# Kernel tuning notes

Hardware: AMD Instinct MI355X
Metric: run time of the kernel (lower is better)

Reference implementation:

```python
import jax, jax.numpy as jnp
import numpy as np

NUM_NODES = 8192
IN_FEATURES = 1024
OUT_FEATURES = 512
NUM_EDGES = 262144  # avg degree 32


def setup_inputs() -> dict:
    key = jax.random.key(0)
    k_x, k_w, k_b, k_src, k_dst = jax.random.split(key, 5)
    x = jax.random.normal(k_x, (NUM_NODES, IN_FEATURES), dtype=jnp.float32)
    # torch nn.Linear layout: weight [out, in], bias [out]
    W = jax.random.normal(k_w, (OUT_FEATURES, IN_FEATURES), dtype=jnp.float32) * (1.0 / np.sqrt(IN_FEATURES))
    b = jax.random.normal(k_b, (OUT_FEATURES,), dtype=jnp.float32) * 0.01
    src = jax.random.randint(k_src, (NUM_EDGES,), 0, NUM_NODES, dtype=jnp.int64)
    dst = jax.random.randint(k_dst, (NUM_EDGES,), 0, NUM_NODES, dtype=jnp.int64)
    edge_index = jnp.stack([src, dst], axis=0)
    return {"x": x, "W": W, "b": b, "edge_index": edge_index, "num_nodes": NUM_NODES}


def reference(x, W, b, edge_index, num_nodes):
    # Faithful to the torch module: build dense adjacency from edge list
    # (duplicate edges collapse to 1.0 via assignment semantics),
    # linear, (dropout p=0 -> identity), dense adj @ hidden, relu.
    adj = jnp.zeros((num_nodes, num_nodes), dtype=x.dtype)
    adj = adj.at[edge_index[0], edge_index[1]].set(1.0)
    hidden = x @ W.T + b            # [N, out]
    support = adj @ hidden          # [N, out] aggregation over neighbors
    return jax.nn.relu(support)
```

## Files before the change

### kernel.cpp

```cpp
#include <hip/hip_runtime.h>

#define N_NODES 8192
#define IN_F    1024
#define OUT_F   512
#define N_EDGES 262144
#define STRIDE  96

#define HID_OFF     0u
#define XB_OFF      8388608u
#define WB_OFF      25165824u
#define DEG_OFF     26214400u
#define COL_OFF     26247168u
#define MAX_DEG     STRIDE

typedef short  bf16x8 __attribute__((ext_vector_type(8)));
typedef float  f32x4  __attribute__((ext_vector_type(4)));

__device__ __forceinline__ unsigned short f2bf(float f) {
    unsigned u = __float_as_uint(f);
    u += 0x7fffu + ((u >> 16) & 1u);
    return (unsigned short)(u >> 16);
}

__device__ __forceinline__ void ld_lds16(const void* g, void* l) {
    __builtin_amdgcn_global_load_lds(
        (const __attribute__((address_space(1))) void*)g,
        (__attribute__((address_space(3))) void*)l, 16, 0, 0);
}

#define NX8 (N_NODES * IN_F / 8)
#define NW8 (OUT_F * IN_F / 8)
__global__ __launch_bounds__(256) void cvt_bf16_all(const float* __restrict__ x,
                                                    const float* __restrict__ w,
                                                    unsigned short* __restrict__ xb,
                                                    int* __restrict__ deg) {
    int i = blockIdx.x * blockDim.x + threadIdx.x;
    if (i < N_NODES) deg[i] = 0;
    if (i >= NX8 + NW8) return;
    const float4* p = (i < NX8) ? ((const float4*)x + (size_t)i * 2)
                                : ((const float4*)w + (size_t)(i - NX8) * 2);
    float4 v0 = p[0], v1 = p[1];
    uint4 o;
    o.x = (unsigned)f2bf(v0.x) | ((unsigned)f2bf(v0.y) << 16);
    o.y = (unsigned)f2bf(v0.z) | ((unsigned)f2bf(v0.w) << 16);
    o.z = (unsigned)f2bf(v1.x) | ((unsigned)f2bf(v1.y) << 16);
    o.w = (unsigned)f2bf(v1.z) | ((unsigned)f2bf(v1.w) << 16);
    *((uint4*)xb + i) = o;
}

__global__ __launch_bounds__(256, 4) void gemm_mfma(const unsigned short* __restrict__ Xb,
                                                    const unsigned short* __restrict__ Wb,
                                                    const float* __restrict__ bias,
                                                    unsigned short* __restrict__ H) {
    __shared__ unsigned short As[64 * 32];
    __shared__ unsigned short Bs[64 * 32];

    const int tid  = threadIdx.x;
    const int lane = tid & 63;
    const int wave = tid >> 6;
    const int row0 = blockIdx.x * 64;
    const int col0 = blockIdx.y * 64;
    const int wm   = (wave & 1) * 32;
    const int wn   = (wave >> 1) * 32;
    const int fm   = lane & 15;
    const int fk   = (lane >> 4) * 8;

    f32x4 acc[2][2];
#pragma unroll
    for (int i = 0; i < 2; ++i)
#pragma unroll
        for (int j = 0; j < 2; ++j) acc[i][j] = (f32x4)0.f;

    const int r0 = tid >> 2, kc0 = (tid & 3) * 8;

    for (int k0 = 0; k0 < IN_F; k0 += 32) {
        ld_lds16(Xb + (size_t)(row0 + r0) * IN_F + k0 + kc0, As + tid * 8);
        ld_lds16(Wb + (size_t)(col0 + r0) * IN_F + k0 + kc0, Bs + tid * 8);
        __syncthreads();

        bf16x8 a[2], b[2];
#pragma unroll
        for (int mi = 0; mi < 2; ++mi)
            a[mi] = *(const bf16x8*)&As[(wm + mi * 16 + fm) * 32 + fk];
#pragma unroll
        for (int ni = 0; ni < 2; ++ni)
            b[ni] = *(const bf16x8*)&Bs[(wn + ni * 16 + fm) * 32 + fk];
#pragma unroll
        for (int mi = 0; mi < 2; ++mi)
#pragma unroll
            for (int ni = 0; ni < 2; ++ni)
                acc[mi][ni] = __builtin_amdgcn_mfma_f32_16x16x32_bf16(
                    a[mi], b[ni], acc[mi][ni], 0, 0, 0);
        __syncthreads();
    }

    const int cm = (lane >> 4) * 4;
#pragma unroll
    for (int ni = 0; ni < 2; ++ni) {
        const int col = col0 + wn + ni * 16 + fm;
        const float bv = bias[col];
#pragma unroll
        for (int mi = 0; mi < 2; ++mi) {
#pragma unroll
            for (int r = 0; r < 4; ++r) {
                const int row = row0 + wm + mi * 16 + cm + r;
                H[(size_t)row * OUT_F + col] = f2bf(acc[mi][ni][r] + bv);
            }
        }
    }
}

__global__ void scatter_direct(const int* __restrict__ src, const int* __restrict__ dst,
                               int* __restrict__ deg, int* __restrict__ col) {
    int e = blockIdx.x * blockDim.x + threadIdx.x;
    if (e >= N_EDGES) return;
    int s = src[e];
    int slot = atomicAdd(&deg[s], 1);
    if (slot < STRIDE) col[s * STRIDE + slot] = dst[e];
}

__global__ __launch_bounds__(256) void aggregate(const unsigned short* __restrict__ H,
                                                 const int* __restrict__ dg,
                                                 const int* __restrict__ col,
                                                 float* __restrict__ out) {
    __shared__ int   nbr[MAX_DEG];
    __shared__ int   uniq[MAX_DEG];
    __shared__ float part[4 * OUT_F];
    __shared__ int   lcnt;
    const int v    = blockIdx.x;
    const int tid  = threadIdx.x;
    const int wave = tid >> 6;
    const int lane = tid & 63;
    int deg = dg[v];
    if (deg > MAX_DEG) deg = MAX_DEG;

    if (tid == 0) lcnt = 0;
    for (int i = tid; i < deg; i += 256) nbr[i] = col[v * STRIDE + i];
    __syncthreads();
    for (int i = tid; i < deg; i += 256) {
        int d = nbr[i];
        bool dup = false;
        for (int j = 0; j < i; ++j)
            if (nbr[j] == d) { dup = true; break; }
        if (!dup) uniq[atomicAdd(&lcnt, 1)] = d;
    }
    __syncthreads();
    const int n  = lcnt;
    const int f0 = lane * 8;

    float a0=0,a1=0,a2=0,a3=0,a4=0,a5=0,a6=0,a7=0;
    int e = wave;
    for (; e + 4 < n; e += 8) {
        uint4 h0 = *(const uint4*)&H[(size_t)uniq[e]     * OUT_F + f0];
        uint4 h1 = *(const uint4*)&H[(size_t)uniq[e + 4] * OUT_F + f0];
        a0 += __uint_as_float(h0.x << 16) + __uint_as_float(h1.x << 16);
        a1 += __uint_as_float(h0.x & 0xffff0000u) + __uint_as_float(h1.x & 0xffff0000u);
        a2 += __uint_as_float(h0.y << 16) + __uint_as_float(h1.y << 16);
        a3 += __uint_as_float(h0.y & 0xffff0000u) + __uint_as_float(h1.y & 0xffff0000u);
        a4 += __uint_as_float(h0.z << 16) + __uint_as_float(h1.z << 16);
        a5 += __uint_as_float(h0.z & 0xffff0000u) + __uint_as_float(h1.z & 0xffff0000u);
        a6 += __uint_as_float(h0.w << 16) + __uint_as_float(h1.w << 16);
        a7 += __uint_as_float(h0.w & 0xffff0000u) + __uint_as_float(h1.w & 0xffff0000u);
    }
    for (; e < n; e += 4) {
        uint4 h0 = *(const uint4*)&H[(size_t)uniq[e] * OUT_F + f0];
        a0 += __uint_as_float(h0.x << 16);
        a1 += __uint_as_float(h0.x & 0xffff0000u);
        a2 += __uint_as_float(h0.y << 16);
        a3 += __uint_as_float(h0.y & 0xffff0000u);
        a4 += __uint_as_float(h0.z << 16);
        a5 += __uint_as_float(h0.z & 0xffff0000u);
        a6 += __uint_as_float(h0.w << 16);
        a7 += __uint_as_float(h0.w & 0xffff0000u);
    }
    float4 p0 = {a0, a1, a2, a3}, p1 = {a4, a5, a6, a7};
    *(float4*)&part[wave * OUT_F + f0]     = p0;
    *(float4*)&part[wave * OUT_F + f0 + 4] = p1;
    __syncthreads();

    const int f = tid * 2;
    float sx = part[0 * OUT_F + f]     + part[1 * OUT_F + f]
             + part[2 * OUT_F + f]     + part[3 * OUT_F + f];
    float sy = part[0 * OUT_F + f + 1] + part[1 * OUT_F + f + 1]
             + part[2 * OUT_F + f + 1] + part[3 * OUT_F + f + 1];
    float2 o;
    o.x = fmaxf(sx, 0.f);
    o.y = fmaxf(sy, 0.f);
    *(float2*)&out[(size_t)v * OUT_F + f] = o;
}

extern "C" void kernel_launch(void* const* d_in, const int* in_sizes, int n_in,
                              void* d_out, int out_size, void* d_ws, size_t ws_size,
                              hipStream_t stream) {
    const float* x  = (const float*)d_in[0];
    const float* W  = (const float*)d_in[1];
    const float* b  = (const float*)d_in[2];
    const int*   ei = (const int*)d_in[3];
    float* out = (float*)d_out;

    char* ws = (char*)d_ws;
    unsigned short* H   = (unsigned short*)(ws + HID_OFF);
    unsigned short* Xb  = (unsigned short*)(ws + XB_OFF);
    unsigned short* Wb  = (unsigned short*)(ws + WB_OFF);
    int*            deg = (int*)(ws + DEG_OFF);
    int*            col = (int*)(ws + COL_OFF);

    cvt_bf16_all<<<(NX8 + NW8 + 255) / 256, 256, 0, stream>>>(x, W, Xb, deg);

    scatter_direct<<<(N_EDGES + 255) / 256, 256, 0, stream>>>(ei, ei + N_EDGES, deg, col);

    gemm_mfma<<<dim3(N_NODES / 64, OUT_F / 64), 256, 0, stream>>>(Xb, Wb, b, H);

    aggregate<<<N_NODES, 256, 0, stream>>>(H, deg, col, out);
}
```

Measured before the change: 154.7 us.

## Fuse edge scatter into GEMM launch and use one wave per node in aggregation

The edge scatter is merged into the GEMM kernel as extra blocks (block ids 1024 and above) on a 1D grid, removing one kernel launch and letting the atomics overlap with MFMA work. The aggregation kernel now assigns one node per wavefront instead of one per block. This replaces block-wide barriers and the LDS cross-wave reduction with wave barriers, and deduplication runs per wave. The risk is less memory-level parallelism per node, with each wave walking all its neighbours serially, plus GEMM and scatter blocks competing for the same compute units.

```diff
diff --git a/kernel.cpp b/kernel.cpp
--- a/kernel.cpp
+++ b/kernel.cpp
@@ -21,6 +21,9 @@
     u += 0x7fffu + ((u >> 16) & 1u);
     return (unsigned short)(u >> 16);
 }
+
+__device__ __forceinline__ float bflo(unsigned u) { return __uint_as_float(u << 16); }
+__device__ __forceinline__ float bfhi(unsigned u) { return __uint_as_float(u & 0xffff0000u); }
 
 __device__ __forceinline__ void ld_lds16(const void* g, void* l) {
     __builtin_amdgcn_global_load_lds(
@@ -48,18 +51,32 @@
     *((uint4*)xb + i) = o;
 }
 
-__global__ __launch_bounds__(256, 4) void gemm_mfma(const unsigned short* __restrict__ Xb,
-                                                    const unsigned short* __restrict__ Wb,
-                                                    const float* __restrict__ bias,
-                                                    unsigned short* __restrict__ H) {
+__global__ __launch_bounds__(256, 4) void gemm_scatter(const unsigned short* __restrict__ Xb,
+                                                       const unsigned short* __restrict__ Wb,
+                                                       const float* __restrict__ bias,
+                                                       unsigned short* __restrict__ H,
+                                                       const int* __restrict__ src,
+                                                       const int* __restrict__ dst,
+                                                       int* __restrict__ deg,
+                                                       int* __restrict__ col) {
     __shared__ unsigned short As[64 * 32];
     __shared__ unsigned short Bs[64 * 32];
 
-    const int tid  = threadIdx.x;
+    const int bid = blockIdx.x;
+    const int tid = threadIdx.x;
+
+    if (bid >= 1024) {
+        int e = (bid - 1024) * 256 + tid;
+        int s = src[e];
+        int slot = atomicAdd(&deg[s], 1);
+        if (slot < STRIDE) col[s * STRIDE + slot] = dst[e];
+        return;
+    }
+
     const int lane = tid & 63;
     const int wave = tid >> 6;
-    const int row0 = blockIdx.x * 64;
-    const int col0 = blockIdx.y * 64;
+    const int row0 = (bid & 127) * 64;
+    const int col0 = (bid >> 7) * 64;
     const int wm   = (wave & 1) * 32;
     const int wn   = (wave >> 1) * 32;
     const int fm   = lane & 15;
@@ -97,96 +114,79 @@
     const int cm = (lane >> 4) * 4;
 #pragma unroll
     for (int ni = 0; ni < 2; ++ni) {
-        const int col = col0 + wn + ni * 16 + fm;
-        const float bv = bias[col];
+        const int c = col0 + wn + ni * 16 + fm;
+        const float bv = bias[c];
 #pragma unroll
         for (int mi = 0; mi < 2; ++mi) {
 #pragma unroll
             for (int r = 0; r < 4; ++r) {
                 const int row = row0 + wm + mi * 16 + cm + r;
-                H[(size_t)row * OUT_F + col] = f2bf(acc[mi][ni][r] + bv);
+                H[(size_t)row * OUT_F + c] = f2bf(acc[mi][ni][r] + bv);
             }
         }
     }
-}
-
-__global__ void scatter_direct(const int* __restrict__ src, const int* __restrict__ dst,
-                               int* __restrict__ deg, int* __restrict__ col) {
-    int e = blockIdx.x * blockDim.x + threadIdx.x;
-    if (e >= N_EDGES) return;
-    int s = src[e];
-    int slot = atomicAdd(&deg[s], 1);
-    if (slot < STRIDE) col[s * STRIDE + slot] = dst[e];
 }
 
 __global__ __launch_bounds__(256) void aggregate(const unsigned short* __restrict__ H,
                                                  const int* __restrict__ dg,
                                                  const int* __restrict__ col,
                                                  float* __restrict__ out) {
-    __shared__ int   nbr[MAX_DEG];
-    __shared__ int   uniq[MAX_DEG];
-    __shared__ float part[4 * OUT_F];
-    __shared__ int   lcnt;
-    const int v    = blockIdx.x;
-    const int tid  = threadIdx.x;
-    const int wave = tid >> 6;
-    const int lane = tid & 63;
-    int deg = dg[v];
-    if (deg > MAX_DEG) deg = MAX_DEG;
-
-    if (tid == 0) lcnt = 0;
-    for (int i = tid; i < deg; i += 256) nbr[i] = col[v * STRIDE + i];
-    __syncthreads();
-    for (int i = tid; i < deg; i += 256) {
-        int d = nbr[i];
-        bool dup = false;
-        for (int j = 0; j < i; ++j)
-            if (nbr[j] == d) { dup = true; break; }
-        if (!dup) uniq[atomicAdd(&lcnt, 1)] = d;
-    }
-    __syncthreads();
-    const int n  = lcnt;
+    __shared__ int nbr[4][MAX_DEG];
+    __shared__ int uniq[4][MAX_DEG];
+    __shared__ int wcnt[4];
+    const int wave = threadIdx.x >> 6;
+    const int lane = threadIdx.x & 63;
+    const int v    = blockIdx.x * 4 + wave;
+    int d = dg[v];
+    if (d > MAX_DEG) d = MAX_DEG;
+
+    if (lane == 0) wcnt[wave] = 0;
+    int id0 = -1, id1 = -1;
+    if (lane < d)      { id0 = col[v * STRIDE + lane];      nbr[wave][lane]      = id0; }
+    if (64 + lane < d) { id1 = col[v * STRIDE + 64 + lane]; nbr[wave][64 + lane] = id1; }
+    __builtin_amdgcn_wave_barrier();
+
+    bool k0 = (lane < d);
+    const int lim0 = k0 ? lane : 0;
+    for (int j = 0; j < lim0; ++j) k0 = k0 & (nbr[wave][j] != id0);
+    bool k1 = (64 + lane < d);
+    const int lim1 = k1 ? (64 + lane) : 0;
+    for (int j = 0; j < lim1; ++j) k1 = k1 & (nbr[wave][j] != id1);
+    if (k0) uniq[wave][atomicAdd(&wcnt[wave], 1)] = id0;
+    if (k1) uniq[wave][atomicAdd(&wcnt[wave], 1)] = id1;
+    __builtin_amdgcn_wave_barrier();
+    const int n  = wcnt[wave];
     const int f0 = lane * 8;
 
     float a0=0,a1=0,a2=0,a3=0,a4=0,a5=0,a6=0,a7=0;
-    int e = wave;
-    for (; e + 4 < n; e += 8) {
-        uint4 h0 = *(const uint4*)&H[(size_t)uniq[e]     * OUT_F + f0];
-        uint4 h1 = *(const uint4*)&H[(size_t)uniq[e + 4] * OUT_F + f0];
-        a0 += __uint_as_float(h0.x << 16) + __uint_as_float(h1.x << 16);
-        a1 += __uint_as_float(h0.x & 0xffff0000u) + __uint_as_float(h1.x & 0xffff0000u);
-        a2 += __uint_as_float(h0.y << 16) + __uint_as_float(h1.y << 16);
-        a3 += __uint_as_float(h0.y & 0xffff0000u) + __uint_as_float(h1.y & 0xffff0000u);
-        a4 += __uint_as_float(h0.z << 16) + __uint_as_float(h1.z << 16);
-        a5 += __uint_as_float(h0.z & 0xffff0000u) + __uint_as_float(h1.z & 0xffff0000u);
-        a6 += __uint_as_float(h0.w << 16) + __uint_as_float(h1.w << 16);
-        a7 += __uint_as_float(h0.w & 0xffff0000u) + __uint_as_float(h1.w & 0xffff0000u);
-    }
-    for (; e < n; e += 4) {
-        uint4 h0 = *(const uint4*)&H[(size_t)uniq[e] * OUT_F + f0];
-        a0 += __uint_as_float(h0.x << 16);
-        a1 += __uint_as_float(h0.x & 0xffff0000u);
-        a2 += __uint_as_float(h0.y << 16);
-        a3 += __uint_as_float(h0.y & 0xffff0000u);
-        a4 += __uint_as_float(h0.z << 16);
-        a5 += __uint_as_float(h0.z & 0xffff0000u);
-        a6 += __uint_as_float(h0.w << 16);
-        a7 += __uint_as_float(h0.w & 0xffff0000u);
-    }
-    float4 p0 = {a0, a1, a2, a3}, p1 = {a4, a5, a6, a7};
-    *(float4*)&part[wave * OUT_F + f0]     = p0;
-    *(float4*)&part[wave * OUT_F + f0 + 4] = p1;
-    __syncthreads();
-
-    const int f = tid * 2;
-    float sx = part[0 * OUT_F + f]     + part[1 * OUT_F + f]
-             + part[2 * OUT_F + f]     + part[3 * OUT_F + f];
-    float sy = part[0 * OUT_F + f + 1] + part[1 * OUT_F + f + 1]
-             + part[2 * OUT_F + f + 1] + part[3 * OUT_F + f + 1];
-    float2 o;
-    o.x = fmaxf(sx, 0.f);
-    o.y = fmaxf(sy, 0.f);
-    *(float2*)&out[(size_t)v * OUT_F + f] = o;
+    int e = 0;
+    for (; e + 4 <= n; e += 4) {
+        const int i0 = uniq[wave][e], i1 = uniq[wave][e+1],
+                  i2 = uniq[wave][e+2], i3 = uniq[wave][e+3];
+        uint4 h0 = *(const uint4*)&H[(size_t)i0 * OUT_F + f0];
+        uint4 h1 = *(const uint4*)&H[(size_t)i1 * OUT_F + f0];
+        uint4 h2 = *(const uint4*)&H[(size_t)i2 * OUT_F + f0];
+        uint4 h3 = *(const uint4*)&H[(size_t)i3 * OUT_F + f0];
+        a0 += bflo(h0.x)+bflo(h1.x)+bflo(h2.x)+bflo(h3.x);
+        a1 += bfhi(h0.x)+bfhi(h1.x)+bfhi(h2.x)+bfhi(h3.x);
+        a2 += bflo(h0.y)+bflo(h1.y)+bflo(h2.y)+bflo(h3.y);
+        a3 += bfhi(h0.y)+bfhi(h1.y)+bfhi(h2.y)+bfhi(h3.y);
+        a4 += bflo(h0.z)+bflo(h1.z)+bflo(h2.z)+bflo(h3.z);
+        a5 += bfhi(h0.z)+bfhi(h1.z)+bfhi(h2.z)+bfhi(h3.z);
+        a6 += bflo(h0.w)+bflo(h1.w)+bflo(h2.w)+bflo(h3.w);
+        a7 += bfhi(h0.w)+bfhi(h1.w)+bfhi(h2.w)+bfhi(h3.w);
+    }
+    for (; e < n; ++e) {
+        uint4 h0 = *(const uint4*)&H[(size_t)uniq[wave][e] * OUT_F + f0];
+        a0 += bflo(h0.x); a1 += bfhi(h0.x);
+        a2 += bflo(h0.y); a3 += bfhi(h0.y);
+        a4 += bflo(h0.z); a5 += bfhi(h0.z);
+        a6 += bflo(h0.w); a7 += bfhi(h0.w);
+    }
+    float4 o0 = {fmaxf(a0,0.f), fmaxf(a1,0.f), fmaxf(a2,0.f), fmaxf(a3,0.f)};
+    float4 o1 = {fmaxf(a4,0.f), fmaxf(a5,0.f), fmaxf(a6,0.f), fmaxf(a7,0.f)};
+    *(float4*)&out[(size_t)v * OUT_F + f0]     = o0;
+    *(float4*)&out[(size_t)v * OUT_F + f0 + 4] = o1;
 }
 
 extern "C" void kernel_launch(void* const* d_in, const int* in_sizes, int n_in,
@@ -207,9 +207,7 @@
 
     cvt_bf16_all<<<(NX8 + NW8 + 255) / 256, 256, 0, stream>>>(x, W, Xb, deg);
 
-    scatter_direct<<<(N_EDGES + 255) / 256, 256, 0, stream>>>(ei, ei + N_EDGES, deg, col);
-
-    gemm_mfma<<<dim3(N_NODES / 64, OUT_F / 64), 256, 0, stream>>>(Xb, Wb, b, H);
-
-    aggregate<<<N_NODES, 256, 0, stream>>>(H, deg, col, out);
-}
+    gemm_scatter<<<2048, 256, 0, stream>>>(Xb, Wb, b, H, ei, ei + N_EDGES, deg, col);
+
+    aggregate<<<N_NODES / 4, 256, 0, stream>>>(H, deg, col, out);
+}
```

Result: faster. 139.5 us (-9.8%).
